# Optimization experiments

Hardware: AMD Instinct MI355X
Metric: run time of the kernel (lower is better)

The kernel has to match this reference:

```python
import jax, jax.numpy as jnp
import numpy as np

N_NODES = 50000
N0, N1 = 30000, 20000
N_EDGES = 600000
NUM_EDGE_TYPES = 8
NUM_NODE_TYPES = 2
IN_C, HID_C, OUT_C = 128, 128, 40


def setup_inputs() -> dict:
    key = jax.random.key(0)
    ks = jax.random.split(key, 12)
    s = 1.0 / np.sqrt(IN_C)
    inp = {
        'x0': jax.random.normal(ks[0], (N0, IN_C), jnp.float32),
        'emb1': jax.random.normal(ks[1], (N1, IN_C), jnp.float32),
        'rel_w1': jax.random.uniform(ks[2], (NUM_EDGE_TYPES, HID_C, IN_C), jnp.float32, -s, s),
        'root_w1': jax.random.uniform(ks[3], (NUM_NODE_TYPES, HID_C, IN_C), jnp.float32, -s, s),
        'root_b1': jax.random.uniform(ks[4], (NUM_NODE_TYPES, HID_C), jnp.float32, -s, s),
        'rel_w2': jax.random.uniform(ks[5], (NUM_EDGE_TYPES, OUT_C, HID_C), jnp.float32, -s, s),
        'root_w2': jax.random.uniform(ks[6], (NUM_NODE_TYPES, OUT_C, HID_C), jnp.float32, -s, s),
        'root_b2': jax.random.uniform(ks[7], (NUM_NODE_TYPES, OUT_C), jnp.float32, -s, s),
        'edge_index': jax.random.randint(ks[8], (2, N_EDGES), 0, N_NODES, jnp.int32),
        'edge_type': jax.random.randint(ks[9], (N_EDGES,), 0, NUM_EDGE_TYPES, jnp.int32),
        # nodes are ordered by type: first N0 of type 0 (featured), then N1 of type 1 (embedded)
        'node_type': jnp.concatenate([jnp.zeros(N0, jnp.int32), jnp.ones(N1, jnp.int32)]),
        'local_node_idx': jnp.concatenate([jnp.arange(N0, dtype=jnp.int32), jnp.arange(N1, dtype=jnp.int32)]),
    }
    return inp


def _group_input(x0, emb1, node_type, local_node_idx):
    mask0 = (node_type == 0)[:, None]
    h0 = x0[jnp.clip(local_node_idx, 0, N0 - 1)]
    h1 = emb1[jnp.clip(local_node_idx, 0, N1 - 1)]
    return jnp.where(mask0, h0, h1)  # [N, IN_C]


def _rgcn_conv(x, edge_index, edge_type, node_type, rel_w, root_w, root_b):
    N = x.shape[0]
    src, dst = edge_index[0], edge_index[1]
    # per-relation transform of all nodes: [T, N, out]
    x_trans = jnp.einsum('nd,tod->tno', x, rel_w)
    msg = x_trans[edge_type, src]  # [E, out] gather by (relation, source)
    # scatter-MEAN per edge type: count edges per (type, dst) segment
    comb = edge_type * N + dst
    cnt = jax.ops.segment_sum(jnp.ones_like(edge_type, dtype=x.dtype), comb,
                              num_segments=NUM_EDGE_TYPES * N)
    denom = jnp.maximum(cnt[comb], 1.0)[:, None]
    out = jax.ops.segment_sum(msg / denom, dst, num_segments=N)
    # masked per-node-type root linears
    for i in range(NUM_NODE_TYPES):
        mask = (node_type == i)[:, None]
        out = out + mask * (x @ root_w[i].T + root_b[i])
    return out


def reference(x0, emb1, rel_w1, root_w1, root_b1, rel_w2, root_w2, root_b2,
              edge_index, edge_type, node_type, local_node_idx):
    x = _group_input(x0, emb1, node_type, local_node_idx)
    x = _rgcn_conv(x, edge_index, edge_type, node_type, rel_w1, root_w1, root_b1)
    x = jax.nn.relu(x)  # dropout identity in eval mode
    x = _rgcn_conv(x, edge_index, edge_type, node_type, rel_w2, root_w2, root_b2)
    return jax.nn.log_softmax(x, axis=-1)
```

## Files before the change

### kernel.cpp

```cpp
#include <hip/hip_runtime.h>

#define NN 50000
#define NN0 30000
#define NN1 20000
#define NE 600000
#define INC 128
#define HIDC 128
#define OUTC 40
#define RS 1152
#define RSB 2304
#define KST 36
#define CAP 64
#define OVCAP 65536
#define XB 3125
#define FB 2344
#define PB 198

typedef __attribute__((ext_vector_type(4))) float f32x4;
typedef __attribute__((ext_vector_type(8))) short s16x8;

static __device__ __forceinline__ unsigned short f2bf(float f){
  unsigned u = __builtin_bit_cast(unsigned, f);
  u = u + 0x7fffu + ((u >> 16) & 1u);
  return (unsigned short)(u >> 16);
}
static __device__ __forceinline__ float bflo(unsigned w){
  return __builtin_bit_cast(float, w << 16);
}
static __device__ __forceinline__ float bfhi(unsigned w){
  return __builtin_bit_cast(float, w & 0xffff0000u);
}

__global__ void build_k(const float* __restrict__ x0, const float* __restrict__ e1,
                        const int* __restrict__ ntp, const int* __restrict__ lix,
                        char* __restrict__ A,
                        const int* __restrict__ ei, const int* __restrict__ et,
                        int* __restrict__ deg, int* __restrict__ eb,
                        int* __restrict__ ovf, int* __restrict__ ovc,
                        const float* __restrict__ rw1, const float* __restrict__ qw1,
                        const float* __restrict__ rw2, const float* __restrict__ qw2,
                        short* __restrict__ Bp1, short* __restrict__ Bp2){
  int b = blockIdx.x;
  if(b < XB){
    int tid = b * 256 + threadIdx.x;
    int n = tid >> 4, q = tid & 15;
    if(n >= NN) return;
    int t = ntp[n], li = lix[n];
    const float* s;
    if(t == 0){ li = li < 0 ? 0 : (li > NN0 - 1 ? NN0 - 1 : li); s = x0 + (size_t)li * INC; }
    else      { li = li < 0 ? 0 : (li > NN1 - 1 ? NN1 - 1 : li); s = e1 + (size_t)li * INC; }
    float4 a = ((const float4*)s)[q * 2];
    float4 c = ((const float4*)s)[q * 2 + 1];
    uint4 o;
    o.x = (unsigned)f2bf(a.x) | ((unsigned)f2bf(a.y) << 16);
    o.y = (unsigned)f2bf(a.z) | ((unsigned)f2bf(a.w) << 16);
    o.z = (unsigned)f2bf(c.x) | ((unsigned)f2bf(c.y) << 16);
    o.w = (unsigned)f2bf(c.z) | ((unsigned)f2bf(c.w) << 16);
    *(uint4*)(A + (size_t)n * RSB + 2048 + q * 16) = o;
    return;
  }
  if(b < XB + FB){
    int e = (b - XB) * 256 + threadIdx.x;
    if(e >= NE) return;
    int s = ei[e], d = ei[NE + e], t = et[e];
    int pos = atomicAdd(&deg[d], 1);
    if(pos < CAP) eb[d * CAP + pos] = s | (t << 16);
    else { int oi = atomicAdd(ovc, 1); if(oi < OVCAP) ovf[oi] = e; }
    return;
  }
  int tid = (b - XB - FB) * 256 + threadIdx.x;
  if(tid < 2 * KST * 8 * 64){
    int l = tid & 63, j = (tid >> 6) & 7, ks = (tid >> 9) % KST, v = (tid >> 9) / KST;
    int n = j * 16 + (l & 15);
    int kb = ks * 32 + (l >> 4) * 8;
    s16x8 ov;
    #pragma unroll
    for(int jj = 0; jj < 8; jj++){
      int k = kb + jj; float wv;
      if(k < 1024){ int t = k >> 7, ki = k & 127; wv = rw1[((size_t)t * HIDC + n) * INC + ki]; }
      else        { wv = qw1[((size_t)v * HIDC + n) * INC + (k - 1024)]; }
      ov[jj] = (short)f2bf(wv);
    }
    ((s16x8*)Bp1)[tid] = ov;
    return;
  }
  int tid2 = tid - 2 * KST * 8 * 64;
  if(tid2 >= 2 * KST * 3 * 64) return;
  int l = tid2 & 63;
  int q = tid2 >> 6;
  int j = q % 3; q /= 3;
  int ks = q % KST, v = q / KST;
  int n = j * 16 + (l & 15);
  int kb = ks * 32 + (l >> 4) * 8;
  s16x8 ov;
  #pragma unroll
  for(int jj = 0; jj < 8; jj++){
    int k = kb + jj; float wv = 0.f;
    if(n < OUTC){
      if(k < 1024){ int t = k >> 7, ki = k & 127; wv = rw2[((size_t)t * OUTC + n) * INC + ki]; }
      else        { wv = qw2[((size_t)v * OUTC + n) * INC + (k - 1024)]; }
    }
    ov[jj] = (short)f2bf(wv);
  }
  ((s16x8*)Bp2)[tid2] = ov;
}

__global__ __launch_bounds__(256) void agg_k(const int* __restrict__ eb, const int* __restrict__ deg,
                                             char* __restrict__ A,
                                             const int* __restrict__ ovf, const int* __restrict__ ovc,
                                             const int* __restrict__ ei, const int* __restrict__ et){
  int wid = (blockIdx.x * 256 + threadIdx.x) >> 6;
  int l = threadIdx.x & 63;
  if(wid >= NN) return;
  int d = __builtin_amdgcn_readfirstlane(wid);
  int dg = deg[d];
  int nb = dg < CAP ? dg : CAP;
  const char* Af = A + 2048;
  int voff = l * 4;
  float acc[16];
  #pragma unroll
  for(int j = 0; j < 16; j++) acc[j] = 0.f;
  int c0 = 0, c1 = 0, c2 = 0, c3 = 0, c4 = 0, c5 = 0, c6 = 0, c7 = 0;

#define ACCUM(T, W) { \
  float fx_ = bflo(W), fy_ = bfhi(W); \
  switch(T){ \
    case 0: acc[0]  += fx_; acc[1]  += fy_; c0++; break; \
    case 1: acc[2]  += fx_; acc[3]  += fy_; c1++; break; \
    case 2: acc[4]  += fx_; acc[5]  += fy_; c2++; break; \
    case 3: acc[6]  += fx_; acc[7]  += fy_; c3++; break; \
    case 4: acc[8]  += fx_; acc[9]  += fy_; c4++; break; \
    case 5: acc[10] += fx_; acc[11] += fy_; c5++; break; \
    case 6: acc[12] += fx_; acc[13] += fy_; c6++; break; \
    default: acc[14] += fx_; acc[15] += fy_; c7++; break; \
  } }

  int base = d * CAP;
  int i = 0;
  for(; i + 3 < nb; i += 4){
    int p0 = eb[base + i + 0];
    int p1 = eb[base + i + 1];
    int p2 = eb[base + i + 2];
    int p3 = eb[base + i + 3];
    unsigned w0 = *(const unsigned*)(Af + (size_t)(p0 & 0xffff) * RSB + voff);
    unsigned w1 = *(const unsigned*)(Af + (size_t)(p1 & 0xffff) * RSB + voff);
    unsigned w2 = *(const unsigned*)(Af + (size_t)(p2 & 0xffff) * RSB + voff);
    unsigned w3 = *(const unsigned*)(Af + (size_t)(p3 & 0xffff) * RSB + voff);
    ACCUM(p0 >> 16, w0);
    ACCUM(p1 >> 16, w1);
    ACCUM(p2 >> 16, w2);
    ACCUM(p3 >> 16, w3);
  }
  for(; i < nb; i++){
    int p0 = eb[base + i];
    unsigned w0 = *(const unsigned*)(Af + (size_t)(p0 & 0xffff) * RSB + voff);
    ACCUM(p0 >> 16, w0);
  }
  if(dg > CAP){
    int oc = *ovc; if(oc > OVCAP) oc = OVCAP;
    for(int k = 0; k < oc; k++){
      int e = ovf[k];
      if(ei[NE + e] != d) continue;
      int s = ei[e];
      int t0 = et[e];
      unsigned w0 = *(const unsigned*)(Af + (size_t)s * RSB + voff);
      ACCUM(t0, w0);
    }
  }
#undef ACCUM

#define STORE(TT, CT) { \
    float iv = 1.0f / (float)((CT) > 1 ? (CT) : 1); \
    unsigned o = (unsigned)f2bf(acc[2*(TT)] * iv) | ((unsigned)f2bf(acc[2*(TT)+1] * iv) << 16); \
    *(unsigned*)(A + (size_t)d * RSB + (TT) * 256 + voff) = o; \
  }
  STORE(0, c0); STORE(1, c1); STORE(2, c2); STORE(3, c3);
  STORE(4, c4); STORE(5, c5); STORE(6, c6); STORE(7, c7);
#undef STORE
}

__global__ __launch_bounds__(256) void gemm1_k(char* __restrict__ A, const s16x8* __restrict__ Bp,
                                               const float* __restrict__ rb, int nb0){
  int b = blockIdx.x;
  int v, rowbase, rowlim;
  if(b < nb0){ v = 0; rowbase = b * 64; rowlim = NN0; }
  else       { v = 1; rowbase = NN0 + (b - nb0) * 64; rowlim = NN; }
  int w = threadIdx.x >> 6, l = threadIdx.x & 63;
  int lm = l & 15, lk = l >> 4;
  int mrow = rowbase + w * 16 + lm;
  int mc = mrow < NN ? mrow : NN - 1;
  const char* arow = A + (size_t)mc * RSB;
  const s16x8* bv = Bp + (size_t)v * (KST * 8 * 64);

  f32x4 acc[8];
  #pragma unroll
  for(int j = 0; j < 8; j++) acc[j] = (f32x4)(0.f);

  for(int ks = 0; ks < KST; ks++){
    s16x8 af = *(const s16x8*)(arow + ks * 64 + lk * 16);
    const s16x8* bk = bv + (size_t)ks * (8 * 64) + l;
    #pragma unroll
    for(int j = 0; j < 8; j++)
      acc[j] = __builtin_amdgcn_mfma_f32_16x16x32_bf16(af, bk[j * 64], acc[j], 0, 0, 0);
  }
  #pragma unroll
  for(int j = 0; j < 8; j++){
    int col = j * 16 + lm;
    float bias = rb[v * HIDC + col];
    #pragma unroll
    for(int r = 0; r < 4; r++){
      int row = rowbase + w * 16 + lk * 4 + r;
      if(row < rowlim){
        float hv = acc[j][r] + bias;
        hv = hv > 0.f ? hv : 0.f;
        *(unsigned short*)(A + (size_t)row * RSB + 2048 + col * 2) = f2bf(hv);
      }
    }
  }
}

__global__ __launch_bounds__(256) void gemm2_k(const char* __restrict__ A, const s16x8* __restrict__ Bp,
                                               const float* __restrict__ rb, float* __restrict__ out, int nb0){
  int b = blockIdx.x;
  int v, rowbase, rowlim;
  if(b < nb0){ v = 0; rowbase = b * 64; rowlim = NN0; }
  else       { v = 1; rowbase = NN0 + (b - nb0) * 64; rowlim = NN; }
  int w = threadIdx.x >> 6, l = threadIdx.x & 63;
  int lm = l & 15, lk = l >> 4;
  int mrow = rowbase + w * 16 + lm;
  int mc = mrow < NN ? mrow : NN - 1;
  const char* arow = A + (size_t)mc * RSB;
  const s16x8* bv = Bp + (size_t)v * (KST * 3 * 64);

  f32x4 acc[3];
  #pragma unroll
  for(int j = 0; j < 3; j++) acc[j] = (f32x4)(0.f);

  for(int ks = 0; ks < KST; ks++){
    s16x8 af = *(const s16x8*)(arow + ks * 64 + lk * 16);
    const s16x8* bk = bv + (size_t)ks * (3 * 64) + l;
    #pragma unroll
    for(int j = 0; j < 3; j++)
      acc[j] = __builtin_amdgcn_mfma_f32_16x16x32_bf16(af, bk[j * 64], acc[j], 0, 0, 0);
  }

  float vals[3][4];
  #pragma unroll
  for(int j = 0; j < 3; j++){
    int col = j * 16 + lm;
    float bias = col < OUTC ? rb[v * OUTC + col] : 0.f;
    #pragma unroll
    for(int r = 0; r < 4; r++) vals[j][r] = acc[j][r] + bias;
  }
  float mx[4], se[4];
  #pragma unroll
  for(int r = 0; r < 4; r++){
    float m = -1e30f;
    #pragma unroll
    for(int j = 0; j < 3; j++) if(j * 16 + lm < OUTC) m = fmaxf(m, vals[j][r]);
    mx[r] = m;
  }
  #pragma unroll
  for(int s = 1; s < 16; s <<= 1){
    #pragma unroll
    for(int r = 0; r < 4; r++) mx[r] = fmaxf(mx[r], __shfl_xor(mx[r], s, 64));
  }
  #pragma unroll
  for(int r = 0; r < 4; r++){
    float a = 0.f;
    #pragma unroll
    for(int j = 0; j < 3; j++) if(j * 16 + lm < OUTC) a += __expf(vals[j][r] - mx[r]);
    se[r] = a;
  }
  #pragma unroll
  for(int s = 1; s < 16; s <<= 1){
    #pragma unroll
    for(int r = 0; r < 4; r++) se[r] += __shfl_xor(se[r], s, 64);
  }
  #pragma unroll
  for(int r = 0; r < 4; r++) se[r] = logf(se[r]);
  #pragma unroll
  for(int j = 0; j < 3; j++){
    int col = j * 16 + lm;
    if(col >= OUTC) continue;
    #pragma unroll
    for(int r = 0; r < 4; r++){
      int row = rowbase + w * 16 + lk * 4 + r;
      if(row < rowlim) out[(size_t)row * OUTC + col] = vals[j][r] - mx[r] - se[r];
    }
  }
}

extern "C" void kernel_launch(void* const* d_in, const int* in_sizes, int n_in,
                              void* d_out, int out_size, void* d_ws, size_t ws_size,
                              hipStream_t stream){
  const float* x0  = (const float*)d_in[0];
  const float* e1  = (const float*)d_in[1];
  const float* rw1 = (const float*)d_in[2];
  const float* qw1 = (const float*)d_in[3];
  const float* qb1 = (const float*)d_in[4];
  const float* rw2 = (const float*)d_in[5];
  const float* qw2 = (const float*)d_in[6];
  const float* qb2 = (const float*)d_in[7];
  const int*   ei  = (const int*)d_in[8];
  const int*   et  = (const int*)d_in[9];
  const int*   ntp = (const int*)d_in[10];
  const int*   lix = (const int*)d_in[11];
  float* out = (float*)d_out;

  const size_t A_OFF   = 0;
  const size_t EB_OFF  = 115200000;
  const size_t DEG_OFF = 128000000;
  const size_t OVC_OFF = 128200000;
  const size_t OVF_OFF = 128200256;
  const size_t BP1_OFF = 128462400;
  const size_t BP2_OFF = 129052224;
  const size_t TOTAL   = 129273408;
  if(ws_size < TOTAL) return;

  char* ws = (char*)d_ws;
  char*  A   = ws + A_OFF;
  int*   eb  = (int*)(ws + EB_OFF);
  int*   deg = (int*)(ws + DEG_OFF);
  int*   ovc = (int*)(ws + OVC_OFF);
  int*   ovf = (int*)(ws + OVF_OFF);
  short* Bp1 = (short*)(ws + BP1_OFF);
  short* Bp2 = (short*)(ws + BP2_OFF);

  int nb0 = (NN0 + 63) / 64;
  int nb1 = (NN - NN0 + 63) / 64;

  hipMemsetAsync(deg, 0, 200000 + 256, stream);
  build_k<<<XB + FB + PB, 256, 0, stream>>>(x0, e1, ntp, lix, A, ei, et, deg, eb, ovf, ovc,
                                            rw1, qw1, rw2, qw2, Bp1, Bp2);
  agg_k<<<(NN * 64 + 255) / 256, 256, 0, stream>>>(eb, deg, A, ovf, ovc, ei, et);
  gemm1_k<<<nb0 + nb1, 256, 0, stream>>>(A, (const s16x8*)Bp1, qb1, nb0);
  agg_k<<<(NN * 64 + 255) / 256, 256, 0, stream>>>(eb, deg, A, ovf, ovc, ei, et);
  gemm2_k<<<nb0 + nb1, 256, 0, stream>>>(A, (const s16x8*)Bp2, qb2, out, nb0);
}
```

Before: 330.1 us.

## Split GEMM K-loop across two wave groups with LDS reduction

Both GEMM kernels now launch 512 threads per block, and the 36-step K loop is split into two halves handled by separate groups of four waves. The upper group writes its partial accumulators to shared memory, and after a barrier the lower group adds them before the bias, ReLU or log-softmax epilogue. This doubles the waves working on each 64-row tile to expose more memory-level parallelism and shorten the serial K chain. In exchange it adds LDS traffic, a block-wide barrier, and half the waves idling during the epilogue.

```diff
diff --git a/kernel.cpp b/kernel.cpp
--- a/kernel.cpp
+++ b/kernel.cpp
@@ -10,6 +10,7 @@
 #define RS 1152
 #define RSB 2304
 #define KST 36
+#define KH 18
 #define CAP 64
 #define OVCAP 65536
 #define XB 3125
@@ -179,78 +180,101 @@
 #undef STORE
 }
 
-__global__ __launch_bounds__(256) void gemm1_k(char* __restrict__ A, const s16x8* __restrict__ Bp,
+__global__ __launch_bounds__(512) void gemm1_k(char* __restrict__ A, const s16x8* __restrict__ Bp,
                                                const float* __restrict__ rb, int nb0){
   int b = blockIdx.x;
   int v, rowbase, rowlim;
   if(b < nb0){ v = 0; rowbase = b * 64; rowlim = NN0; }
   else       { v = 1; rowbase = NN0 + (b - nb0) * 64; rowlim = NN; }
   int w = threadIdx.x >> 6, l = threadIdx.x & 63;
+  int rg = w & 3, kh = w >> 2;
   int lm = l & 15, lk = l >> 4;
-  int mrow = rowbase + w * 16 + lm;
-  int mc = mrow < NN ? mrow : NN - 1;
-  const char* arow = A + (size_t)mc * RSB;
-  const s16x8* bv = Bp + (size_t)v * (KST * 8 * 64);
+  int mrow = rowbase + rg * 16 + lm;
+  const char* arow = A + (size_t)(mrow < NN ? mrow : NN - 1) * RSB;
+  const s16x8* bv = Bp + (size_t)v * (KST * 8 * 64) + l;
 
   f32x4 acc[8];
   #pragma unroll
   for(int j = 0; j < 8; j++) acc[j] = (f32x4)(0.f);
 
-  for(int ks = 0; ks < KST; ks++){
+  int ks0 = kh * KH;
+  #pragma unroll 2
+  for(int ks = ks0; ks < ks0 + KH; ks++){
     s16x8 af = *(const s16x8*)(arow + ks * 64 + lk * 16);
-    const s16x8* bk = bv + (size_t)ks * (8 * 64) + l;
+    const s16x8* bk = bv + (size_t)ks * (8 * 64);
     #pragma unroll
     for(int j = 0; j < 8; j++)
       acc[j] = __builtin_amdgcn_mfma_f32_16x16x32_bf16(af, bk[j * 64], acc[j], 0, 0, 0);
   }
-  #pragma unroll
-  for(int j = 0; j < 8; j++){
-    int col = j * 16 + lm;
-    float bias = rb[v * HIDC + col];
-    #pragma unroll
-    for(int r = 0; r < 4; r++){
-      int row = rowbase + w * 16 + lk * 4 + r;
-      if(row < rowlim){
-        float hv = acc[j][r] + bias;
-        hv = hv > 0.f ? hv : 0.f;
-        *(unsigned short*)(A + (size_t)row * RSB + 2048 + col * 2) = f2bf(hv);
+
+  __shared__ f32x4 red[4][8][64];
+  if(kh == 1){
+    #pragma unroll
+    for(int j = 0; j < 8; j++) red[rg][j][l] = acc[j];
+  }
+  __syncthreads();
+  if(kh == 0){
+    #pragma unroll
+    for(int j = 0; j < 8; j++){
+      f32x4 o = red[rg][j][l];
+      int col = j * 16 + lm;
+      float bias = rb[v * HIDC + col];
+      #pragma unroll
+      for(int r = 0; r < 4; r++){
+        int row = rowbase + rg * 16 + lk * 4 + r;
+        if(row < rowlim){
+          float hv = acc[j][r] + o[r] + bias;
+          hv = hv > 0.f ? hv : 0.f;
+          *(unsigned short*)(A + (size_t)row * RSB + 2048 + col * 2) = f2bf(hv);
+        }
       }
     }
   }
 }
 
-__global__ __launch_bounds__(256) void gemm2_k(const char* __restrict__ A, const s16x8* __restrict__ Bp,
+__global__ __launch_bounds__(512) void gemm2_k(const char* __restrict__ A, const s16x8* __restrict__ Bp,
                                                const float* __restrict__ rb, float* __restrict__ out, int nb0){
   int b = blockIdx.x;
   int v, rowbase, rowlim;
   if(b < nb0){ v = 0; rowbase = b * 64; rowlim = NN0; }
   else       { v = 1; rowbase = NN0 + (b - nb0) * 64; rowlim = NN; }
   int w = threadIdx.x >> 6, l = threadIdx.x & 63;
+  int rg = w & 3, kh = w >> 2;
   int lm = l & 15, lk = l >> 4;
-  int mrow = rowbase + w * 16 + lm;
-  int mc = mrow < NN ? mrow : NN - 1;
-  const char* arow = A + (size_t)mc * RSB;
-  const s16x8* bv = Bp + (size_t)v * (KST * 3 * 64);
+  int mrow = rowbase + rg * 16 + lm;
+  const char* arow = A + (size_t)(mrow < NN ? mrow : NN - 1) * RSB;
+  const s16x8* bv = Bp + (size_t)v * (KST * 3 * 64) + l;
 
   f32x4 acc[3];
   #pragma unroll
   for(int j = 0; j < 3; j++) acc[j] = (f32x4)(0.f);
 
-  for(int ks = 0; ks < KST; ks++){
+  int ks0 = kh * KH;
+  #pragma unroll 2
+  for(int ks = ks0; ks < ks0 + KH; ks++){
     s16x8 af = *(const s16x8*)(arow + ks * 64 + lk * 16);
-    const s16x8* bk = bv + (size_t)ks * (3 * 64) + l;
+    const s16x8* bk = bv + (size_t)ks * (3 * 64);
     #pragma unroll
     for(int j = 0; j < 3; j++)
       acc[j] = __builtin_amdgcn_mfma_f32_16x16x32_bf16(af, bk[j * 64], acc[j], 0, 0, 0);
   }
+
+  __shared__ f32x4 red[4][3][64];
+  if(kh == 1){
+    #pragma unroll
+    for(int j = 0; j < 3; j++) red[rg][j][l] = acc[j];
+  }
+  __syncthreads();
+  if(kh != 0) return;
 
   float vals[3][4];
   #pragma unroll
   for(int j = 0; j < 3; j++){
     int col = j * 16 + lm;
     float bias = col < OUTC ? rb[v * OUTC + col] : 0.f;
-    #pragma unroll
-    for(int r = 0; r < 4; r++) vals[j][r] = acc[j][r] + bias;
+    f32x4 o = red[rg][j][l];
+    #pragma unroll
+    for(int r = 0; r < 4; r++) vals[j][r] = acc[j][r] + o[r] + bias;
   }
   float mx[4], se[4];
   #pragma unroll
@@ -285,7 +309,7 @@
     if(col >= OUTC) continue;
     #pragma unroll
     for(int r = 0; r < 4; r++){
-      int row = rowbase + w * 16 + lk * 4 + r;
+      int row = rowbase + rg * 16 + lk * 4 + r;
       if(row < rowlim) out[(size_t)row * OUTC + col] = vals[j][r] - mx[r] - se[r];
     }
   }
@@ -334,7 +358,7 @@
   build_k<<<XB + FB + PB, 256, 0, stream>>>(x0, e1, ntp, lix, A, ei, et, deg, eb, ovf, ovc,
                                             rw1, qw1, rw2, qw2, Bp1, Bp2);
   agg_k<<<(NN * 64 + 255) / 256, 256, 0, stream>>>(eb, deg, A, ovf, ovc, ei, et);
-  gemm1_k<<<nb0 + nb1, 256, 0, stream>>>(A, (const s16x8*)Bp1, qb1, nb0);
+  gemm1_k<<<nb0 + nb1, 512, 0, stream>>>(A, (const s16x8*)Bp1, qb1, nb0);
   agg_k<<<(NN * 64 + 255) / 256, 256, 0, stream>>>(eb, deg, A, ovf, ovc, ei, et);
-  gemm2_k<<<nb0 + nb1, 256, 0, stream>>>(A, (const s16x8*)Bp2, qb2, out, nb0);
-}
+  gemm2_k<<<nb0 + nb1, 512, 0, stream>>>(A, (const s16x8*)Bp2, qb2, out, nb0);
+}
```

After: 334.0 us. No clear change (+1.2%).

## Stage GEMM tiles through LDS with double-buffered direct global-to-LDS loads

Applied to the files above, without the earlier changes.

Both GEMM kernels now use 128-row tiles and 512 threads. Each k-step of A and packed B is staged into shared memory with global_load_lds, double-buffered so the next step's load overlaps the MFMAs on the current one. B fragments are shared by the waves of a block instead of each wave reading them from global memory, and gemm1 gives each wave a 32x64 output tile for register-level reuse. The cost is a barrier every k-step and fewer, larger blocks.

```diff
diff --git a/kernel.cpp b/kernel.cpp
--- a/kernel.cpp
+++ b/kernel.cpp
@@ -7,7 +7,6 @@
 #define INC 128
 #define HIDC 128
 #define OUTC 40
-#define RS 1152
 #define RSB 2304
 #define KST 36
 #define CAP 64
@@ -29,6 +28,11 @@
 }
 static __device__ __forceinline__ float bfhi(unsigned w){
   return __builtin_bit_cast(float, w & 0xffff0000u);
+}
+static __device__ __forceinline__ void gll16(const void* g, void* l){
+  __builtin_amdgcn_global_load_lds(
+    (const __attribute__((address_space(1))) unsigned int*)g,
+    (__attribute__((address_space(3))) unsigned int*)l, 16, 0, 0);
 }
 
 __global__ void build_k(const float* __restrict__ x0, const float* __restrict__ e1,
@@ -179,69 +183,114 @@
 #undef STORE
 }
 
-__global__ __launch_bounds__(256) void gemm1_k(char* __restrict__ A, const s16x8* __restrict__ Bp,
+__global__ __launch_bounds__(512) void gemm1_k(char* __restrict__ A, const char* __restrict__ Bp,
                                                const float* __restrict__ rb, int nb0){
+  __shared__ char lds[32768];
   int b = blockIdx.x;
   int v, rowbase, rowlim;
-  if(b < nb0){ v = 0; rowbase = b * 64; rowlim = NN0; }
-  else       { v = 1; rowbase = NN0 + (b - nb0) * 64; rowlim = NN; }
-  int w = threadIdx.x >> 6, l = threadIdx.x & 63;
-  int lm = l & 15, lk = l >> 4;
-  int mrow = rowbase + w * 16 + lm;
-  int mc = mrow < NN ? mrow : NN - 1;
-  const char* arow = A + (size_t)mc * RSB;
-  const s16x8* bv = Bp + (size_t)v * (KST * 8 * 64);
-
-  f32x4 acc[8];
-  #pragma unroll
-  for(int j = 0; j < 8; j++) acc[j] = (f32x4)(0.f);
-
+  if(b < nb0){ v = 0; rowbase = b * 128; rowlim = NN0; }
+  else       { v = 1; rowbase = NN0 + (b - nb0) * 128; rowlim = NN; }
+  int t = threadIdx.x, w = t >> 6, l = t & 63;
+  int wr = w >> 1, wc = w & 1, lm = l & 15, lk = l >> 4;
+
+  int srow = rowbase + (t & 127);
+  if(srow > NN - 1) srow = NN - 1;
+  const char* asrc = A + (size_t)srow * RSB + (t >> 7) * 16;
+  const char* bsrc = Bp + (size_t)v * 294912 + t * 16;
+  char* adst = lds + t * 16;
+  char* bdst = lds + 16384 + t * 16;
+
+  f32x4 acc[2][4];
+  #pragma unroll
+  for(int rf = 0; rf < 2; rf++)
+    #pragma unroll
+    for(int cf = 0; cf < 4; cf++) acc[rf][cf] = (f32x4)(0.f);
+
+  gll16(asrc, adst);
+  gll16(bsrc, bdst);
+  __syncthreads();
+  int cur = 0;
+  #pragma unroll 1
   for(int ks = 0; ks < KST; ks++){
-    s16x8 af = *(const s16x8*)(arow + ks * 64 + lk * 16);
-    const s16x8* bk = bv + (size_t)ks * (8 * 64) + l;
-    #pragma unroll
-    for(int j = 0; j < 8; j++)
-      acc[j] = __builtin_amdgcn_mfma_f32_16x16x32_bf16(af, bk[j * 64], acc[j], 0, 0, 0);
-  }
-  #pragma unroll
-  for(int j = 0; j < 8; j++){
-    int col = j * 16 + lm;
+    int nxt = cur ^ 1;
+    if(ks + 1 < KST){
+      gll16(asrc + (ks + 1) * 64, adst + nxt * 8192);
+      gll16(bsrc + (size_t)(ks + 1) * 8192, bdst + nxt * 8192);
+    }
+    const char* ab = lds + cur * 8192;
+    const char* bb = lds + 16384 + cur * 8192;
+    s16x8 a0 = *(const s16x8*)(ab + (lk * 128 + wr * 32 + lm) * 16);
+    s16x8 a1 = *(const s16x8*)(ab + (lk * 128 + wr * 32 + 16 + lm) * 16);
+    #pragma unroll
+    for(int cf = 0; cf < 4; cf++){
+      s16x8 bj = *(const s16x8*)(bb + ((wc * 4 + cf) * 64 + l) * 16);
+      acc[0][cf] = __builtin_amdgcn_mfma_f32_16x16x32_bf16(a0, bj, acc[0][cf], 0, 0, 0);
+      acc[1][cf] = __builtin_amdgcn_mfma_f32_16x16x32_bf16(a1, bj, acc[1][cf], 0, 0, 0);
+    }
+    __syncthreads();
+    cur = nxt;
+  }
+  #pragma unroll
+  for(int cf = 0; cf < 4; cf++){
+    int col = (wc * 4 + cf) * 16 + lm;
     float bias = rb[v * HIDC + col];
     #pragma unroll
-    for(int r = 0; r < 4; r++){
-      int row = rowbase + w * 16 + lk * 4 + r;
-      if(row < rowlim){
-        float hv = acc[j][r] + bias;
-        hv = hv > 0.f ? hv : 0.f;
-        *(unsigned short*)(A + (size_t)row * RSB + 2048 + col * 2) = f2bf(hv);
+    for(int rf = 0; rf < 2; rf++){
+      #pragma unroll
+      for(int r = 0; r < 4; r++){
+        int row = rowbase + wr * 32 + rf * 16 + lk * 4 + r;
+        if(row < rowlim){
+          float hv = acc[rf][cf][r] + bias;
+          hv = hv > 0.f ? hv : 0.f;
+          *(unsigned short*)(A + (size_t)row * RSB + 2048 + col * 2) = f2bf(hv);
+        }
       }
     }
   }
 }
 
-__global__ __launch_bounds__(256) void gemm2_k(const char* __restrict__ A, const s16x8* __restrict__ Bp,
+__global__ __launch_bounds__(512) void gemm2_k(const char* __restrict__ A, const char* __restrict__ Bp,
                                                const float* __restrict__ rb, float* __restrict__ out, int nb0){
+  __shared__ char lds[22528];
   int b = blockIdx.x;
   int v, rowbase, rowlim;
-  if(b < nb0){ v = 0; rowbase = b * 64; rowlim = NN0; }
-  else       { v = 1; rowbase = NN0 + (b - nb0) * 64; rowlim = NN; }
-  int w = threadIdx.x >> 6, l = threadIdx.x & 63;
+  if(b < nb0){ v = 0; rowbase = b * 128; rowlim = NN0; }
+  else       { v = 1; rowbase = NN0 + (b - nb0) * 128; rowlim = NN; }
+  int t = threadIdx.x, w = t >> 6, l = t & 63;
   int lm = l & 15, lk = l >> 4;
-  int mrow = rowbase + w * 16 + lm;
-  int mc = mrow < NN ? mrow : NN - 1;
-  const char* arow = A + (size_t)mc * RSB;
-  const s16x8* bv = Bp + (size_t)v * (KST * 3 * 64);
+
+  int srow = rowbase + (t & 127);
+  if(srow > NN - 1) srow = NN - 1;
+  const char* asrc = A + (size_t)srow * RSB + (t >> 7) * 16;
+  const char* bsrc = Bp + (size_t)v * 110592 + t * 16;
+  char* adst = lds + t * 16;
+  char* bdst = lds + 16384 + t * 16;
 
   f32x4 acc[3];
   #pragma unroll
   for(int j = 0; j < 3; j++) acc[j] = (f32x4)(0.f);
 
+  gll16(asrc, adst);
+  if(w < 3) gll16(bsrc, bdst);
+  __syncthreads();
+  int cur = 0;
+  #pragma unroll 1
   for(int ks = 0; ks < KST; ks++){
-    s16x8 af = *(const s16x8*)(arow + ks * 64 + lk * 16);
-    const s16x8* bk = bv + (size_t)ks * (3 * 64) + l;
-    #pragma unroll
-    for(int j = 0; j < 3; j++)
-      acc[j] = __builtin_amdgcn_mfma_f32_16x16x32_bf16(af, bk[j * 64], acc[j], 0, 0, 0);
+    int nxt = cur ^ 1;
+    if(ks + 1 < KST){
+      gll16(asrc + (ks + 1) * 64, adst + nxt * 8192);
+      if(w < 3) gll16(bsrc + (size_t)(ks + 1) * 3072, bdst + nxt * 3072);
+    }
+    const char* ab = lds + cur * 8192;
+    const char* bb = lds + 16384 + cur * 3072;
+    s16x8 af = *(const s16x8*)(ab + (lk * 128 + w * 16 + lm) * 16);
+    #pragma unroll
+    for(int j = 0; j < 3; j++){
+      s16x8 bj = *(const s16x8*)(bb + (j * 64 + l) * 16);
+      acc[j] = __builtin_amdgcn_mfma_f32_16x16x32_bf16(af, bj, acc[j], 0, 0, 0);
+    }
+    __syncthreads();
+    cur = nxt;
   }
 
   float vals[3][4];
@@ -327,14 +376,14 @@
   short* Bp1 = (short*)(ws + BP1_OFF);
   short* Bp2 = (short*)(ws + BP2_OFF);
 
-  int nb0 = (NN0 + 63) / 64;
-  int nb1 = (NN - NN0 + 63) / 64;
+  int nb0 = (NN0 + 127) / 128;
+  int nb1 = (NN - NN0 + 127) / 128;
 
   hipMemsetAsync(deg, 0, 200000 + 256, stream);
   build_k<<<XB + FB + PB, 256, 0, stream>>>(x0, e1, ntp, lix, A, ei, et, deg, eb, ovf, ovc,
                                             rw1, qw1, rw2, qw2, Bp1, Bp2);
   agg_k<<<(NN * 64 + 255) / 256, 256, 0, stream>>>(eb, deg, A, ovf, ovc, ei, et);
-  gemm1_k<<<nb0 + nb1, 256, 0, stream>>>(A, (const s16x8*)Bp1, qb1, nb0);
+  gemm1_k<<<nb0 + nb1, 512, 0, stream>>>(A, (const char*)Bp1, qb1, nb0);
   agg_k<<<(NN * 64 + 255) / 256, 256, 0, stream>>>(eb, deg, A, ovf, ovc, ei, et);
-  gemm2_k<<<nb0 + nb1, 256, 0, stream>>>(A, (const s16x8*)Bp2, qb2, out, nb0);
-}
+  gemm2_k<<<nb0 + nb1, 512, 0, stream>>>(A, (const char*)Bp2, qb2, out, nb0);
+}
```

New measurement: 304.7 us. 7.7% less time.
